# Performance work log

Measured on AMD Instinct MI355X. Metric: run time of the kernel, lower is better.

The kernel has to match this reference:

```python
import jax, jax.numpy as jnp
import numpy as np

H = 768
NH = 12
HD = H // NH
FF = 3072
EPS = 1e-5
CHUNK = 32  # query chunk for L1 distance to bound memory


def layer_norm(x, g, b):
    mu = jnp.mean(x, axis=-1, keepdims=True)
    var = jnp.mean((x - mu) ** 2, axis=-1, keepdims=True)
    return (x - mu) / jnp.sqrt(var + EPS) * g + b


def l1_distance(Q, K):
    # Q, K: [BH, S, D] -> [BH, S, S], computed in query chunks to avoid
    # materializing the full [BH, S, S, D] broadcast intermediate.
    BH, S, D = Q.shape
    nc = S // CHUNK
    Qc = Q.reshape(BH, nc, CHUNK, D).transpose(1, 0, 2, 3)  # [nc, BH, c, D]

    def f(qc):  # qc: [BH, c, D]
        return jnp.sum(jnp.abs(qc[:, :, None, :] - K[:, None, :, :]), axis=-1)

    d = jax.lax.map(f, Qc)  # [nc, BH, c, S]
    return d.transpose(1, 0, 2, 3).reshape(BH, S, S)


def setup_inputs() -> dict:
    key = jax.random.key(0)
    ks = jax.random.split(key, 12)
    sd = 0.02
    B, S = 2, 1024
    return {
        'hidden_states': jax.random.normal(ks[0], (B, S, H), jnp.float32),
        'ln1_g': jnp.ones((H,), jnp.float32),
        'ln1_b': jnp.zeros((H,), jnp.float32),
        'Wq': jax.random.normal(ks[1], (H, H), jnp.float32) * sd,
        'bq': jnp.zeros((H,), jnp.float32),
        'Wk': jax.random.normal(ks[2], (H, H), jnp.float32) * sd,
        'bk': jnp.zeros((H,), jnp.float32),
        'Wv': jax.random.normal(ks[3], (H, H), jnp.float32) * sd,
        'bv': jnp.zeros((H,), jnp.float32),
        'Wo': jax.random.normal(ks[4], (H, H), jnp.float32) * sd,
        'bo': jnp.zeros((H,), jnp.float32),
        'lam': jnp.asarray(1.0, jnp.float32),
        'ln2_g': jnp.ones((H,), jnp.float32),
        'ln2_b': jnp.zeros((H,), jnp.float32),
        'W1': jax.random.normal(ks[5], (H, FF), jnp.float32) * sd,
        'b1': jnp.zeros((FF,), jnp.float32),
        'W2': jax.random.normal(ks[6], (FF, H), jnp.float32) * sd,
        'b2': jnp.zeros((H,), jnp.float32),
    }


def reference(hidden_states, ln1_g, ln1_b, Wq, bq, Wk, bk, Wv, bv, Wo, bo,
              lam, ln2_g, ln2_b, W1, b1, W2, b2):
    B, S, _ = hidden_states.shape
    scale = 1.0 / np.sqrt(HD)

    residual = hidden_states
    x = layer_norm(hidden_states, ln1_g, ln1_b)

    Q = (x @ Wq + bq).reshape(B, S, NH, HD).transpose(0, 2, 1, 3)  # [B,H,S,D]
    K = (x @ Wk + bk).reshape(B, S, NH, HD).transpose(0, 2, 1, 3)
    V = (x @ Wv + bv).reshape(B, S, NH, HD).transpose(0, 2, 1, 3)

    Qf = Q.reshape(B * NH, S, HD)
    Kf = K.reshape(B * NH, S, HD)
    dist = l1_distance(Qf, Kf).reshape(B, NH, S, S)

    scores = -lam * dist * scale
    attn = jax.nn.softmax(scores, axis=-1)  # [B,H,S,S]

    out = jnp.einsum('bhqk,bhkd->bhqd', attn, V)
    out = out.transpose(0, 2, 1, 3).reshape(B, S, H)
    out = out @ Wo + bo
    out = residual + out

    residual = out
    y = layer_norm(out, ln2_g, ln2_b)
    y = jax.nn.gelu(y @ W1 + b1, approximate=False) @ W2 + b2
    out = residual + y
    return out, attn
```

## Files before the change

### kernel.cpp

```cpp
#include <hip/hip_runtime.h>
#include <cstdint>
#include <cstddef>

#define SB    1024
#define BB    2
#define HH    768
#define NHH   12
#define HDD   64
#define FFF   3072
#define RR    (BB*SB)
#define NQKV  2304

#define QSCALE 42.5f

typedef __attribute__((ext_vector_type(8))) short short8;
typedef __attribute__((ext_vector_type(4))) float f4;

__device__ __forceinline__ unsigned short f2bf(float f) {
  union { float f; unsigned u; } x; x.f = f;
  unsigned r = x.u + 0x7FFFu + ((x.u >> 16) & 1u);
  return (unsigned short)(r >> 16);
}

__device__ __forceinline__ unsigned qz8(float x) {
  int v = (int)rintf(x * QSCALE) + 128;
  v = v < 0 ? 0 : (v > 255 ? 255 : v);
  return (unsigned)v;
}

__device__ __forceinline__ void async16(void* lds, const void* g) {
  __builtin_amdgcn_global_load_lds((const __attribute__((address_space(1))) unsigned int*)g,
                                   (__attribute__((address_space(3))) unsigned int*)lds,
                                   16, 0, 0);
}

__global__ __launch_bounds__(256)
void prep_all(const float* __restrict__ Wq, const float* __restrict__ Wk,
              const float* __restrict__ Wv, const float* __restrict__ Wo,
              const float* __restrict__ W1, const float* __restrict__ W2,
              const float* __restrict__ bq, const float* __restrict__ bk,
              const float* __restrict__ bv,
              const float* __restrict__ hidden, const float* __restrict__ ln1_g,
              const float* __restrict__ ln1_b,
              unsigned short* __restrict__ Wqkv_t, unsigned short* __restrict__ W1t,
              unsigned short* __restrict__ W2t, float* __restrict__ bqkv,
              unsigned short* __restrict__ xb) {
  const int t = blockIdx.x;
  const int tid = threadIdx.x;
  __shared__ float tile[64][65];
  __shared__ float rs[4], rq[4];
  if (t >= 1737) {
    const int row = t - 1737;
    const float* x = hidden + (size_t)row * HH;
    float v0 = x[tid], v1 = x[tid + 256], v2 = x[tid + 512];
    float s = v0 + v1 + v2;
    float q = v0 * v0 + v1 * v1 + v2 * v2;
    #pragma unroll
    for (int o = 32; o >= 1; o >>= 1) { s += __shfl_xor(s, o); q += __shfl_xor(q, o); }
    const int w = tid >> 6;
    if ((tid & 63) == 0) { rs[w] = s; rq[w] = q; }
    __syncthreads();
    s = rs[0] + rs[1] + rs[2] + rs[3];
    q = rq[0] + rq[1] + rq[2] + rq[3];
    float mean = s * (1.0f / HH);
    float rstd = rsqrtf(q * (1.0f / HH) - mean * mean + 1e-5f);
    unsigned short* o0 = xb + (size_t)row * HH;
    o0[tid]       = f2bf((v0 - mean) * rstd * ln1_g[tid]       + ln1_b[tid]);
    o0[tid + 256] = f2bf((v1 - mean) * rstd * ln1_g[tid + 256] + ln1_b[tid + 256]);
    o0[tid + 512] = f2bf((v2 - mean) * rstd * ln1_g[tid + 512] + ln1_b[tid + 512]);
    return;
  }
  if (t >= 1728) {
    int i = (t - 1728) * 256 + tid;
    if (i < NQKV)
      bqkv[i] = (i < HH) ? bq[i] : (i < 2 * HH ? bk[i - HH] : bv[i - 2 * HH]);
    return;
  }
  const float* in; unsigned short* out; int ldin, ldout, r0, c0;
  if (t < 576) {
    int m = t / 144, q = t % 144;
    in = m == 0 ? Wq : (m == 1 ? Wk : (m == 2 ? Wv : Wo));
    out = Wqkv_t + (size_t)m * HH * HH;
    ldin = HH; ldout = HH;
    r0 = (q / 12) * 64; c0 = (q % 12) * 64;
  } else if (t < 1152) {
    int q = t - 576;
    in = W1; out = W1t; ldin = FFF; ldout = HH;
    r0 = (q % 12) * 64; c0 = (q / 12) * 64;
  } else {
    int q = t - 1152;
    in = W2; out = W2t; ldin = HH; ldout = FFF;
    r0 = (q % 48) * 64; c0 = (q / 48) * 64;
  }
  for (int i = tid; i < 4096; i += 256) {
    int r = i >> 6, c = i & 63;
    tile[r][c] = in[(size_t)(r0 + r) * ldin + c0 + c];
  }
  __syncthreads();
  for (int i = tid; i < 4096; i += 256) {
    int cc = i >> 6, rr = i & 63;
    out[(size_t)(c0 + cc) * ldout + r0 + rr] = f2bf(tile[rr][cc]);
  }
}

__global__ __launch_bounds__(256)
void gemm_qkv(const unsigned short* __restrict__ A, const unsigned short* __restrict__ Bt,
              const float* __restrict__ bqkv, unsigned* __restrict__ Qq,
              unsigned* __restrict__ Kq, unsigned short* __restrict__ Vt) {
  __shared__ __align__(16) unsigned char smem[49152];
  unsigned short (*lA)[128 * 32] = (unsigned short (*)[128 * 32])smem;
  unsigned short (*lB)[128 * 32] = (unsigned short (*)[128 * 32])(smem + 24576);
  const unsigned short* Ab = A + (size_t)blockIdx.y * 128 * HH;
  const unsigned short* Bb = Bt + (size_t)blockIdx.x * 128 * HH;
  const int tid = threadIdx.x;
  const int wave = tid >> 6, lane = tid & 63;
  const int wr = wave >> 1, wc = wave & 1;
  const int lo = lane & 15, hi = lane >> 4;

  auto stage = [&](int k0, int buf) {
    #pragma unroll
    for (int i = 0; i < 512; i += 256) {
      int idx = i + tid; int r = idx >> 2, kg = idx & 3;
      async16(&lA[buf][idx * 8], &Ab[(size_t)r * HH + k0 + kg * 8]);
    }
    #pragma unroll
    for (int i = 0; i < 512; i += 256) {
      int idx = i + tid; int r = idx >> 2, kg = idx & 3;
      async16(&lB[buf][idx * 8], &Bb[(size_t)r * HH + k0 + kg * 8]);
    }
  };

  stage(0, 0);
  stage(32, 1);
  f4 acc[4][4] = {};
  for (int it = 0; it < 24; it++) {
    if (it + 1 < 24) {
      asm volatile("s_waitcnt vmcnt(4)" ::: "memory");
    } else {
      asm volatile("s_waitcnt vmcnt(0)" ::: "memory");
    }
    __builtin_amdgcn_s_barrier();
    __builtin_amdgcn_sched_barrier(0);
    const int cur = it % 3;
    short8 af[4], bf[4];
    #pragma unroll
    for (int i = 0; i < 4; i++)
      af[i] = *(const short8*)&lA[cur][(wr * 64 + i * 16 + lo) * 32 + hi * 8];
    #pragma unroll
    for (int j = 0; j < 4; j++)
      bf[j] = *(const short8*)&lB[cur][(wc * 64 + j * 16 + lo) * 32 + hi * 8];
    if (it + 2 < 24) stage((it + 2) * 32, (it + 2) % 3);
    #pragma unroll
    for (int i = 0; i < 4; i++)
      #pragma unroll
      for (int j = 0; j < 4; j++)
        acc[i][j] = __builtin_amdgcn_mfma_f32_16x16x32_bf16(af[i], bf[j], acc[i][j], 0, 0, 0);
  }
  __syncthreads();

  const int reg = blockIdx.x / 6;
  const int cb = blockIdx.x * 128;
  if (reg < 2) {
    unsigned char* t8 = smem;
    #pragma unroll
    for (int i = 0; i < 4; i++)
      #pragma unroll
      for (int j = 0; j < 4; j++) {
        int col = wc * 64 + j * 16 + lo;
        float bv_ = bqkv[cb + col];
        #pragma unroll
        for (int r = 0; r < 4; r++) {
          int row = wr * 64 + i * 16 + hi * 4 + r;
          t8[row * 132 + col] = (unsigned char)qz8(acc[i][j][r] + bv_);
        }
      }
    __syncthreads();
    const unsigned* t32 = (const unsigned*)smem;
    if (reg == 0) {
      #pragma unroll
      for (int i0 = 0; i0 < 4096; i0 += 256) {
        int idx = i0 + tid;
        int cw = idx & 31, rw = idx >> 5;
        int token = blockIdx.y * 128 + rw;
        Qq[(size_t)token * 192 + blockIdx.x * 32 + cw] = t32[rw * 33 + cw];
      }
    } else {
      #pragma unroll
      for (int i0 = 0; i0 < 4096; i0 += 256) {
        int idx = i0 + tid;
        int rw = idx & 127, cw = idx >> 7;
        int token = blockIdx.y * 128 + rw;
        int b = token >> 10, k = token & 1023;
        int dgG = (blockIdx.x - 6) * 32 + cw;
        Kq[(size_t)((b * NHH + (dgG >> 4)) * 16 + (dgG & 15)) * SB + k] = t32[rw * 33 + cw];
      }
    }
  } else {
    unsigned short* t16 = (unsigned short*)smem;
    #pragma unroll
    for (int i = 0; i < 4; i++)
      #pragma unroll
      for (int j = 0; j < 4; j++) {
        int col = wc * 64 + j * 16 + lo;
        float bv_ = bqkv[cb + col];
        #pragma unroll
        for (int r = 0; r < 4; r++) {
          int row = wr * 64 + i * 16 + hi * 4 + r;
          t16[col * 130 + row] = f2bf(acc[i][j][r] + bv_);
        }
      }
    __syncthreads();
    const unsigned* tv = (const unsigned*)smem;
    unsigned* VtU = (unsigned*)Vt;
    #pragma unroll
    for (int i0 = 0; i0 < 8192; i0 += 256) {
      int idx = i0 + tid;
      int rp = idx & 63, cw = idx >> 6;
      int gcol = (blockIdx.x - 12) * 128 + cw;
      int h = gcol >> 6, d = gcol & 63;
      int b = blockIdx.y >> 3;
      VtU[(size_t)((b * NHH + h) * HDD + d) * 512 + (blockIdx.y & 7) * 64 + rp] =
          tv[cw * 65 + rp];
    }
  }
}

template<int BM, int BN, int WR, int WC, int MODE, int KS>
__global__ __launch_bounds__(WR*WC*64)
void gemm_bt(const unsigned short* __restrict__ A, int ldA,
             const unsigned short* __restrict__ Bt, int ldB,
             void* __restrict__ Cv, int ldC,
             const float* __restrict__ bias,
             int K, long partStride) {
  constexpr int T = WR * WC * 64;
  constexpr int LPT = (BM * 4 + BN * 4) / T;
  __shared__ unsigned short lA[3][BM * 32];
  __shared__ unsigned short lB[3][BN * 32];
  const int ks = blockIdx.z;
  const int KH = K / KS;
  const unsigned short* Ab = A + (size_t)blockIdx.y * BM * ldA + (size_t)ks * KH;
  const unsigned short* Bb = Bt + (size_t)blockIdx.x * BN * ldB + (size_t)ks * KH;
  const long cOff = (long)blockIdx.y * BM * ldC + (long)blockIdx.x * BN
                  + (long)ks * partStride;
  const int tid = threadIdx.x;
  const int wave = tid >> 6, lane = tid & 63;
  const int wr = wave / WC, wc = wave % WC;
  const int lo = lane & 15, hi = lane >> 4;

  auto stage = [&](int k0, int buf) {
    #pragma unroll
    for (int i = 0; i < BM * 4; i += T) {
      int idx = i + tid; int r = idx >> 2, kg = idx & 3;
      async16(&lA[buf][idx * 8], &Ab[(size_t)r * ldA + k0 + kg * 8]);
    }
    #pragma unroll
    for (int i = 0; i < BN * 4; i += T) {
      int idx = i + tid; int r = idx >> 2, kg = idx & 3;
      async16(&lB[buf][idx * 8], &Bb[(size_t)r * ldB + k0 + kg * 8]);
    }
  };

  const int nIter = KH / 32;
  stage(0, 0);
  if (nIter > 1) stage(32, 1);
  f4 acc[4][4] = {};
  for (int it = 0; it < nIter; it++) {
    if (it + 1 < nIter) {
      asm volatile("s_waitcnt vmcnt(%0)" :: "n"(LPT) : "memory");
    } else {
      asm volatile("s_waitcnt vmcnt(0)" ::: "memory");
    }
    __builtin_amdgcn_s_barrier();
    __builtin_amdgcn_sched_barrier(0);
    const int cur = it % 3;
    short8 af[4], bf[4];
    #pragma unroll
    for (int i = 0; i < 4; i++)
      af[i] = *(const short8*)&lA[cur][(wr * 64 + i * 16 + lo) * 32 + hi * 8];
    #pragma unroll
    for (int j = 0; j < 4; j++)
      bf[j] = *(const short8*)&lB[cur][(wc * 64 + j * 16 + lo) * 32 + hi * 8];
    if (it + 2 < nIter) stage((it + 2) * 32, (it + 2) % 3);
    #pragma unroll
    for (int i = 0; i < 4; i++)
      #pragma unroll
      for (int j = 0; j < 4; j++)
        acc[i][j] = __builtin_amdgcn_mfma_f32_16x16x32_bf16(af[i], bf[j], acc[i][j], 0, 0, 0);
  }
  float* Cf = (float*)Cv;
  unsigned short* Cb = (unsigned short*)Cv;
  const int bc0 = blockIdx.x * BN;
  #pragma unroll
  for (int i = 0; i < 4; i++) {
    #pragma unroll
    for (int j = 0; j < 4; j++) {
      int col = wc * 64 + j * 16 + lo;
      #pragma unroll
      for (int r = 0; r < 4; r++) {
        int row = wr * 64 + i * 16 + hi * 4 + r;
        size_t idx = (size_t)cOff + (size_t)row * ldC + col;
        float v = acc[i][j][r];
        if constexpr (MODE == 3) {
          float tt = v + bias[bc0 + col];
          Cb[idx] = f2bf(0.5f * tt * (1.0f + erff(tt * 0.70710678118654752f)));
        } else {
          Cf[idx] = v;
        }
      }
    }
  }
}

__global__ __launch_bounds__(256)
void reduce_ln(const float* __restrict__ p, const float* __restrict__ bias,
               const float* __restrict__ res, const float* __restrict__ g,
               const float* __restrict__ bb, float* __restrict__ attnOut,
               unsigned short* __restrict__ out) {
  const int row = blockIdx.x, tid = threadIdx.x;
  const size_t rb = (size_t)row * HH;
  float v[3]; float s = 0.f, q = 0.f;
  #pragma unroll
  for (int j = 0; j < 3; j++) {
    int c = tid + j * 256;
    size_t idx = rb + c;
    float a = p[idx] + p[(size_t)RR * HH + idx] + p[2 * (size_t)RR * HH + idx]
            + p[3 * (size_t)RR * HH + idx] + bias[c] + res[idx];
    attnOut[idx] = a;
    v[j] = a; s += a; q += a * a;
  }
  #pragma unroll
  for (int o = 32; o >= 1; o >>= 1) { s += __shfl_xor(s, o); q += __shfl_xor(q, o); }
  __shared__ float rs[4], rq[4];
  const int w = tid >> 6;
  if ((tid & 63) == 0) { rs[w] = s; rq[w] = q; }
  __syncthreads();
  s = rs[0] + rs[1] + rs[2] + rs[3];
  q = rq[0] + rq[1] + rq[2] + rq[3];
  float mean = s * (1.0f / HH);
  float rstd = rsqrtf(q * (1.0f / HH) - mean * mean + 1e-5f);
  #pragma unroll
  for (int j = 0; j < 3; j++) {
    int c = tid + j * 256;
    out[rb + c] = f2bf((v[j] - mean) * rstd * g[c] + bb[c]);
  }
}

__global__ __launch_bounds__(256)
void reduce4_bias_res(const float* __restrict__ p, const float* __restrict__ bias,
                      const float* __restrict__ res, float* __restrict__ out) {
  int i = (blockIdx.x * 256 + threadIdx.x) * 4;
  int col = i % HH;
  float4 a = *(const float4*)(p + i);
  #pragma unroll
  for (int s = 1; s < 4; s++) {
    float4 b = *(const float4*)(p + (size_t)s * RR * HH + i);
    a.x += b.x; a.y += b.y; a.z += b.z; a.w += b.w;
  }
  float4 bb = *(const float4*)(bias + col);
  float4 r = *(const float4*)(res + i);
  float4 o;
  o.x = a.x + bb.x + r.x;
  o.y = a.y + bb.y + r.y;
  o.z = a.z + bb.z + r.z;
  o.w = a.w + bb.w + r.w;
  *(float4*)(out + i) = o;
}

#define DQ 16
__global__ __launch_bounds__(512)
void dist_softmax_pv(const unsigned* __restrict__ Qq, const unsigned* __restrict__ Kq,
                     const unsigned short* __restrict__ Vt,
                     const float* __restrict__ lam_p,
                     float* __restrict__ attnF, unsigned short* __restrict__ ctx) {
  __shared__ __align__(16) unsigned short lp[DQ * SB];
  __shared__ unsigned lq[DQ * 16];
  const int bh = blockIdx.y;
  const int q0 = blockIdx.x * DQ;
  const int b = bh / NHH, h = bh % NHH;
  const int tid = threadIdx.x;
  const int w = tid >> 6, lane = tid & 63;
  const int lo = lane & 15, hi = lane >> 4;

  if (tid < 256) {
    int r = tid >> 4, dg = tid & 15;
    lq[r * 16 + dg] = Qq[(size_t)(b * SB + q0 + r) * 192 + h * 16 + dg];
  }
  __syncthreads();

  const unsigned* Ks = Kq + (size_t)bh * 16 * SB;
  unsigned acc[2][4][4] = {};
  const unsigned* lqw = &lq[(w * 2) * 16];

  #pragma unroll
  for (int dg = 0; dg < 16; dg++) {
    unsigned qd0 = lqw[dg];
    unsigned qd1 = lqw[16 + dg];
    uint4 kv[4];
    #pragma unroll
    for (int kg = 0; kg < 4; kg++)
      kv[kg] = *(const uint4*)&Ks[(size_t)dg * SB + kg * 256 + lane * 4];
    #pragma unroll
    for (int kg = 0; kg < 4; kg++) {
      acc[0][kg][0] = __builtin_amdgcn_sad_u8(qd0, kv[kg].x, acc[0][kg][0]);
      acc[0][kg][1] = __builtin_amdgcn_sad_u8(qd0, kv[kg].y, acc[0][kg][1]);
      acc[0][kg][2] = __builtin_amdgcn_sad_u8(qd0, kv[kg].z, acc[0][kg][2]);
      acc[0][kg][3] = __builtin_amdgcn_sad_u8(qd0, kv[kg].w, acc[0][kg][3]);
      acc[1][kg][0] = __builtin_amdgcn_sad_u8(qd1, kv[kg].x, acc[1][kg][0]);
      acc[1][kg][1] = __builtin_amdgcn_sad_u8(qd1, kv[kg].y, acc[1][kg][1]);
      acc[1][kg][2] = __builtin_amdgcn_sad_u8(qd1, kv[kg].z, acc[1][kg][2]);
      acc[1][kg][3] = __builtin_amdgcn_sad_u8(qd1, kv[kg].w, acc[1][kg][3]);
    }
  }

  const float kscl = -lam_p[0] * 0.125f / QSCALE;
  #pragma unroll
  for (int qi = 0; qi < 2; qi++) {
    float sc[16];
    float m = -1e30f;
    #pragma unroll
    for (int kg = 0; kg < 4; kg++)
      #pragma unroll
      for (int c = 0; c < 4; c++) {
        float v = (float)acc[qi][kg][c] * kscl;
        sc[kg * 4 + c] = v;
        m = fmaxf(m, v);
      }
    #pragma unroll
    for (int off = 1; off < 64; off <<= 1) m = fmaxf(m, __shfl_xor(m, off));
    float s = 0.f;
    #pragma unroll
    for (int i = 0; i < 16; i++) {
      float e = __expf(sc[i] - m);
      sc[i] = e;
      s += e;
    }
    #pragma unroll
    for (int off = 1; off < 64; off <<= 1) s += __shfl_xor(s, off);
    const float rinv = 1.0f / s;
    const int row = w * 2 + qi;
    const unsigned swz = (unsigned)((row & 7) << 3);
    const size_t gb = (size_t)bh * SB * SB + (size_t)(q0 + row) * SB + lane * 4;
    #pragma unroll
    for (int kg = 0; kg < 4; kg++) {
      float4 p;
      p.x = sc[kg * 4 + 0] * rinv;
      p.y = sc[kg * 4 + 1] * rinv;
      p.z = sc[kg * 4 + 2] * rinv;
      p.w = sc[kg * 4 + 3] * rinv;
      *(float4*)&attnF[gb + kg * 256] = p;
      ushort4 pb;
      pb.x = f2bf(p.x); pb.y = f2bf(p.y); pb.z = f2bf(p.z); pb.w = f2bf(p.w);
      *(ushort4*)&lp[(unsigned)(row * SB + kg * 256 + lane * 4) ^ swz] = pb;
    }
  }
  __syncthreads();

  if (w < 4) {
    const unsigned short* Vb = Vt + ((size_t)bh * HDD + w * 16 + lo) * SB + hi * 8;
    const unsigned pswz = (unsigned)((lo & 7) << 3);
    const unsigned pbase = (unsigned)(lo * SB + hi * 8);
    f4 cacc = {0.f, 0.f, 0.f, 0.f};
    #pragma unroll
    for (int k0 = 0; k0 < SB; k0 += 32) {
      short8 af = *(const short8*)&lp[(pbase + k0) ^ pswz];
      short8 bf = *(const short8*)(Vb + k0);
      cacc = __builtin_amdgcn_mfma_f32_16x16x32_bf16(af, bf, cacc, 0, 0, 0);
    }
    unsigned short* cb = ctx + (size_t)(b * SB + q0 + hi * 4) * HH + h * HDD + w * 16 + lo;
    #pragma unroll
    for (int r = 0; r < 4; r++) cb[(size_t)r * HH] = f2bf(cacc[r]);
  }
}

extern "C" void kernel_launch(void* const* d_in, const int* in_sizes, int n_in,
                              void* d_out, int out_size, void* d_ws, size_t ws_size,
                              hipStream_t stream) {
  (void)in_sizes; (void)n_in; (void)out_size; (void)ws_size;
  const float* hidden = (const float*)d_in[0];
  const float* ln1_g  = (const float*)d_in[1];
  const float* ln1_b  = (const float*)d_in[2];
  const float* Wq     = (const float*)d_in[3];
  const float* bq     = (const float*)d_in[4];
  const float* Wk     = (const float*)d_in[5];
  const float* bk     = (const float*)d_in[6];
  const float* Wv     = (const float*)d_in[7];
  const float* bv     = (const float*)d_in[8];
  const float* Wo     = (const float*)d_in[9];
  const float* bo     = (const float*)d_in[10];
  const float* lam    = (const float*)d_in[11];
  const float* ln2_g  = (const float*)d_in[12];
  const float* ln2_b  = (const float*)d_in[13];
  const float* W1     = (const float*)d_in[14];
  const float* b1     = (const float*)d_in[15];
  const float* W2     = (const float*)d_in[16];
  const float* b2     = (const float*)d_in[17];

  float* out0  = (float*)d_out;
  float* attnF = out0 + (size_t)RR * HH;

  char* w = (char*)d_ws;
  auto alloc = [&](size_t bytes) { char* p = w; w += (bytes + 255) & ~(size_t)255; return p; };
  unsigned short* xb      = (unsigned short*)alloc((size_t)RR * HH * 2);
  unsigned short* Wqkv_t  = (unsigned short*)alloc((size_t)NQKV * HH * 2);
  unsigned short* Wo_t    = (unsigned short*)alloc((size_t)HH * HH * 2);
  unsigned short* W1t     = (unsigned short*)alloc((size_t)FFF * HH * 2);
  unsigned short* W2t     = (unsigned short*)alloc((size_t)HH * FFF * 2);
  float*          bqkv    = (float*)alloc((size_t)NQKV * 4);
  unsigned*       Qq      = (unsigned*)alloc((size_t)RR * 192 * 4);
  unsigned*       Kq      = (unsigned*)alloc((size_t)BB * NHH * 16 * SB * 4);
  unsigned short* Vt      = (unsigned short*)alloc((size_t)BB * NHH * HDD * SB * 2);
  unsigned short* ctx     = (unsigned short*)alloc((size_t)RR * HH * 2);
  float*          attnOut = (float*)alloc((size_t)RR * HH * 4);
  unsigned short* h1      = (unsigned short*)alloc((size_t)RR * FFF * 2);
  float*          gPart   = (float*)alloc((size_t)4 * RR * HH * 4);
  unsigned short* y2      = Vt;
  (void)Wo_t;

  prep_all<<<dim3(1737 + RR), 256, 0, stream>>>(Wq, Wk, Wv, Wo, W1, W2, bq, bk, bv,
                                                hidden, ln1_g, ln1_b,
                                                Wqkv_t, W1t, W2t, bqkv, xb);

  gemm_qkv<<<dim3(NQKV / 128, RR / 128), 256, 0, stream>>>(
      xb, Wqkv_t, bqkv, Qq, Kq, Vt);

  dist_softmax_pv<<<dim3(SB / DQ, BB * NHH), 512, 0, stream>>>(
      Qq, Kq, Vt, lam, attnF, ctx);

  gemm_bt<128, 128, 2, 2, 4, 4><<<dim3(HH / 128, RR / 128, 4), 256, 0, stream>>>(
      ctx, HH, Wqkv_t + (size_t)3 * HH * HH, HH, gPart, HH,
      nullptr, HH, (long)RR * HH);

  reduce_ln<<<dim3(RR), 256, 0, stream>>>(gPart, bo, hidden, ln2_g, ln2_b,
                                          attnOut, y2);

  gemm_bt<128, 128, 2, 2, 3, 1><<<dim3(FFF / 128, RR / 128, 1), 256, 0, stream>>>(
      y2, HH, W1t, HH, h1, FFF, b1, HH, 0);

  gemm_bt<128, 128, 2, 2, 4, 4><<<dim3(HH / 128, RR / 128, 4), 256, 0, stream>>>(
      h1, FFF, W2t, FFF, gPart, HH, nullptr, FFF, (long)RR * HH);

  reduce4_bias_res<<<dim3(RR * HH / 1024), 256, 0, stream>>>(gPart, b2, attnOut, out0);
}
```

Baseline: 294.5 us.

## Split keys across waves in L1-distance softmax, with cross-wave reductions through shared memory

Each wave now owns a 128-key slice for all 16 query rows instead of two query rows over all 1024 keys. K is loaded into registers once per thread, so each K element is read once per block rather than eight times. Q is broadcast from LDS. Row max and row sum now need cross-wave reductions through a small shared array and two extra barriers. The attention-probability stores become narrower float2 writes that each cover 16 rows.

```diff
diff --git a/kernel.cpp b/kernel.cpp
--- a/kernel.cpp
+++ b/kernel.cpp
@@ -374,6 +374,7 @@
                      float* __restrict__ attnF, unsigned short* __restrict__ ctx) {
   __shared__ __align__(16) unsigned short lp[DQ * SB];
   __shared__ unsigned lq[DQ * 16];
+  __shared__ __align__(16) float red[2][DQ][8];
   const int bh = blockIdx.y;
   const int q0 = blockIdx.x * DQ;
   const int b = bh / NHH, h = bh % NHH;
@@ -385,73 +386,83 @@
     int r = tid >> 4, dg = tid & 15;
     lq[r * 16 + dg] = Qq[(size_t)(b * SB + q0 + r) * 192 + h * 16 + dg];
   }
-  __syncthreads();
-
-  const unsigned* Ks = Kq + (size_t)bh * 16 * SB;
-  unsigned acc[2][4][4] = {};
-  const unsigned* lqw = &lq[(w * 2) * 16];
-
-  #pragma unroll
-  for (int dg = 0; dg < 16; dg++) {
-    unsigned qd0 = lqw[dg];
-    unsigned qd1 = lqw[16 + dg];
-    uint4 kv[4];
-    #pragma unroll
-    for (int kg = 0; kg < 4; kg++)
-      kv[kg] = *(const uint4*)&Ks[(size_t)dg * SB + kg * 256 + lane * 4];
-    #pragma unroll
-    for (int kg = 0; kg < 4; kg++) {
-      acc[0][kg][0] = __builtin_amdgcn_sad_u8(qd0, kv[kg].x, acc[0][kg][0]);
-      acc[0][kg][1] = __builtin_amdgcn_sad_u8(qd0, kv[kg].y, acc[0][kg][1]);
-      acc[0][kg][2] = __builtin_amdgcn_sad_u8(qd0, kv[kg].z, acc[0][kg][2]);
-      acc[0][kg][3] = __builtin_amdgcn_sad_u8(qd0, kv[kg].w, acc[0][kg][3]);
-      acc[1][kg][0] = __builtin_amdgcn_sad_u8(qd1, kv[kg].x, acc[1][kg][0]);
-      acc[1][kg][1] = __builtin_amdgcn_sad_u8(qd1, kv[kg].y, acc[1][kg][1]);
-      acc[1][kg][2] = __builtin_amdgcn_sad_u8(qd1, kv[kg].z, acc[1][kg][2]);
-      acc[1][kg][3] = __builtin_amdgcn_sad_u8(qd1, kv[kg].w, acc[1][kg][3]);
-    }
-  }
+
+  const unsigned* Ks = Kq + (size_t)bh * 16 * SB + w * 128 + lane * 2;
+  uint2 kd[16];
+  #pragma unroll
+  for (int dg = 0; dg < 16; dg++)
+    kd[dg] = *(const uint2*)&Ks[(size_t)dg * SB];
+  __syncthreads();
 
   const float kscl = -lam_p[0] * 0.125f / QSCALE;
-  #pragma unroll
-  for (int qi = 0; qi < 2; qi++) {
-    float sc[16];
-    float m = -1e30f;
-    #pragma unroll
-    for (int kg = 0; kg < 4; kg++)
-      #pragma unroll
-      for (int c = 0; c < 4; c++) {
-        float v = (float)acc[qi][kg][c] * kscl;
-        sc[kg * 4 + c] = v;
-        m = fmaxf(m, v);
-      }
+  float sc0[16], sc1[16];
+  #pragma unroll
+  for (int r = 0; r < 16; r++) {
+    uint4 qa = *(const uint4*)&lq[r * 16];
+    uint4 qb = *(const uint4*)&lq[r * 16 + 4];
+    uint4 qc = *(const uint4*)&lq[r * 16 + 8];
+    uint4 qd = *(const uint4*)&lq[r * 16 + 12];
+    unsigned a0 = 0, a1 = 0;
+    a0 = __builtin_amdgcn_sad_u8(qa.x, kd[0].x, a0);  a1 = __builtin_amdgcn_sad_u8(qa.x, kd[0].y, a1);
+    a0 = __builtin_amdgcn_sad_u8(qa.y, kd[1].x, a0);  a1 = __builtin_amdgcn_sad_u8(qa.y, kd[1].y, a1);
+    a0 = __builtin_amdgcn_sad_u8(qa.z, kd[2].x, a0);  a1 = __builtin_amdgcn_sad_u8(qa.z, kd[2].y, a1);
+    a0 = __builtin_amdgcn_sad_u8(qa.w, kd[3].x, a0);  a1 = __builtin_amdgcn_sad_u8(qa.w, kd[3].y, a1);
+    a0 = __builtin_amdgcn_sad_u8(qb.x, kd[4].x, a0);  a1 = __builtin_amdgcn_sad_u8(qb.x, kd[4].y, a1);
+    a0 = __builtin_amdgcn_sad_u8(qb.y, kd[5].x, a0);  a1 = __builtin_amdgcn_sad_u8(qb.y, kd[5].y, a1);
+    a0 = __builtin_amdgcn_sad_u8(qb.z, kd[6].x, a0);  a1 = __builtin_amdgcn_sad_u8(qb.z, kd[6].y, a1);
+    a0 = __builtin_amdgcn_sad_u8(qb.w, kd[7].x, a0);  a1 = __builtin_amdgcn_sad_u8(qb.w, kd[7].y, a1);
+    a0 = __builtin_amdgcn_sad_u8(qc.x, kd[8].x, a0);  a1 = __builtin_amdgcn_sad_u8(qc.x, kd[8].y, a1);
+    a0 = __builtin_amdgcn_sad_u8(qc.y, kd[9].x, a0);  a1 = __builtin_amdgcn_sad_u8(qc.y, kd[9].y, a1);
+    a0 = __builtin_amdgcn_sad_u8(qc.z, kd[10].x, a0); a1 = __builtin_amdgcn_sad_u8(qc.z, kd[10].y, a1);
+    a0 = __builtin_amdgcn_sad_u8(qc.w, kd[11].x, a0); a1 = __builtin_amdgcn_sad_u8(qc.w, kd[11].y, a1);
+    a0 = __builtin_amdgcn_sad_u8(qd.x, kd[12].x, a0); a1 = __builtin_amdgcn_sad_u8(qd.x, kd[12].y, a1);
+    a0 = __builtin_amdgcn_sad_u8(qd.y, kd[13].x, a0); a1 = __builtin_amdgcn_sad_u8(qd.y, kd[13].y, a1);
+    a0 = __builtin_amdgcn_sad_u8(qd.z, kd[14].x, a0); a1 = __builtin_amdgcn_sad_u8(qd.z, kd[14].y, a1);
+    a0 = __builtin_amdgcn_sad_u8(qd.w, kd[15].x, a0); a1 = __builtin_amdgcn_sad_u8(qd.w, kd[15].y, a1);
+    sc0[r] = (float)a0 * kscl;
+    sc1[r] = (float)a1 * kscl;
+  }
+
+  #pragma unroll
+  for (int r = 0; r < 16; r++) {
+    float m = fmaxf(sc0[r], sc1[r]);
     #pragma unroll
     for (int off = 1; off < 64; off <<= 1) m = fmaxf(m, __shfl_xor(m, off));
-    float s = 0.f;
-    #pragma unroll
-    for (int i = 0; i < 16; i++) {
-      float e = __expf(sc[i] - m);
-      sc[i] = e;
-      s += e;
-    }
+    if (lane == 0) red[0][r][w] = m;
+  }
+  __syncthreads();
+
+  float mx[16];
+  #pragma unroll
+  for (int r = 0; r < 16; r++) {
+    float4 a = *(const float4*)&red[0][r][0];
+    float4 c = *(const float4*)&red[0][r][4];
+    mx[r] = fmaxf(fmaxf(fmaxf(a.x, a.y), fmaxf(a.z, a.w)),
+                  fmaxf(fmaxf(c.x, c.y), fmaxf(c.z, c.w)));
+  }
+  #pragma unroll
+  for (int r = 0; r < 16; r++) {
+    sc0[r] = __expf(sc0[r] - mx[r]);
+    sc1[r] = __expf(sc1[r] - mx[r]);
+    float s = sc0[r] + sc1[r];
     #pragma unroll
     for (int off = 1; off < 64; off <<= 1) s += __shfl_xor(s, off);
-    const float rinv = 1.0f / s;
-    const int row = w * 2 + qi;
-    const unsigned swz = (unsigned)((row & 7) << 3);
-    const size_t gb = (size_t)bh * SB * SB + (size_t)(q0 + row) * SB + lane * 4;
-    #pragma unroll
-    for (int kg = 0; kg < 4; kg++) {
-      float4 p;
-      p.x = sc[kg * 4 + 0] * rinv;
-      p.y = sc[kg * 4 + 1] * rinv;
-      p.z = sc[kg * 4 + 2] * rinv;
-      p.w = sc[kg * 4 + 3] * rinv;
-      *(float4*)&attnF[gb + kg * 256] = p;
-      ushort4 pb;
-      pb.x = f2bf(p.x); pb.y = f2bf(p.y); pb.z = f2bf(p.z); pb.w = f2bf(p.w);
-      *(ushort4*)&lp[(unsigned)(row * SB + kg * 256 + lane * 4) ^ swz] = pb;
-    }
+    if (lane == 0) red[1][r][w] = s;
+  }
+  __syncthreads();
+
+  const size_t gbase = (size_t)bh * SB * SB + (size_t)q0 * SB + w * 128 + lane * 2;
+  #pragma unroll
+  for (int r = 0; r < 16; r++) {
+    float4 a = *(const float4*)&red[1][r][0];
+    float4 c = *(const float4*)&red[1][r][4];
+    float rinv = 1.0f / (a.x + a.y + a.z + a.w + c.x + c.y + c.z + c.w);
+    float p0 = sc0[r] * rinv, p1 = sc1[r] * rinv;
+    float2 pw; pw.x = p0; pw.y = p1;
+    *(float2*)&attnF[gbase + (size_t)r * SB] = pw;
+    unsigned pk = (unsigned)f2bf(p0) | ((unsigned)f2bf(p1) << 16);
+    unsigned idx = (unsigned)(r * SB + w * 128 + lane * 2) ^ (unsigned)((r & 7) << 3);
+    *(unsigned*)&lp[idx] = pk;
   }
   __syncthreads();
 
```

Result: slower. 394.4 us (+33.9%).
